# Kernel tuning notes

Measured on AMD Instinct MI355X. Metric: run time of the kernel, lower is better.

Reference implementation:

```python
import jax, jax.numpy as jnp
import numpy as np

N_PREV = 250_000   # rows of `features` / `coors` (voxels at previous scale)
N_FULL = 500_000   # full raw points (coors_inv_full / scale_coors_inv length)
V = 65_536         # voxels at current scale
C_IN = 64
C_OUT = 64
SCALE = 2
EPS = 1e-5


def lrelu(x):
    return jnp.where(x > 0, x, 0.1 * x)


def masked_bn(x, mask, gamma, beta):
    # training-mode BatchNorm1d over valid (non-padded) rows only; mask: [M,1]
    n = jnp.maximum(mask.sum(), 1.0)
    mu = (x * mask).sum(0) / n
    var = (((x - mu) * mask) ** 2).sum(0) / n  # biased var, as torch BN
    return gamma * (x - mu) * jax.lax.rsqrt(var + EPS) + beta


def setup_inputs():
    key = jax.random.key(0)
    ks = jax.random.split(key, 16)
    features = jax.random.normal(ks[0], (N_PREV, C_IN), jnp.float32)
    batch = jax.random.randint(ks[1], (N_PREV, 1), 0, 4)
    xy = jax.random.randint(ks[2], (N_PREV, 2), 0, 1000)
    z = jax.random.randint(ks[3], (N_PREV, 1), 0, 60)
    coors = jnp.concatenate([batch, xy, z], axis=1).astype(jnp.int32)
    coors_inv_full = jax.random.randint(ks[4], (N_FULL,), 0, N_PREV, jnp.int32)
    scale_coors_inv = jax.random.randint(ks[5], (N_FULL,), 0, V, jnp.int32)

    def lin(k, i, o):
        return jax.random.normal(k, (i, o), jnp.float32) / np.sqrt(i).astype(np.float32)

    h = C_OUT // 2
    return dict(
        features=features, coors=coors, coors_inv_full=coors_inv_full,
        scale_coors_inv=scale_coors_inv,
        W_in=lin(ks[6], C_IN, C_OUT), b_in=jnp.zeros((C_OUT,), jnp.float32),
        W1=lin(ks[7], C_IN, h), b1=jnp.zeros((h,), jnp.float32),
        g1=jnp.ones((h,), jnp.float32), be1=jnp.zeros((h,), jnp.float32),
        W2=lin(ks[8], h, h), b2=jnp.zeros((h,), jnp.float32),
        g2=jnp.ones((h,), jnp.float32), be2=jnp.zeros((h,), jnp.float32),
        W3=lin(ks[9], h, C_OUT), b3=jnp.zeros((C_OUT,), jnp.float32),
        Wo1=lin(ks[10], 2 * C_OUT, C_OUT), bo1=jnp.zeros((C_OUT,), jnp.float32),
        Wo2=lin(ks[11], C_OUT, C_OUT), bo2=jnp.zeros((C_OUT,), jnp.float32),
    )


def reference(features, coors, coors_inv_full, scale_coors_inv,
              W_in, b_in, W1, b1, g1, be1, W2, b2, g2, be2, W3, b3,
              Wo1, bo1, Wo2, bo2):
    # --- downsample: unique voxel key + scatter_mean (torch.unique return_inverse) ---
    b = coors[:, 0].astype(jnp.int32)
    xyz = coors[:, 1:].astype(jnp.int32) // SCALE
    keys = ((b * 501 + xyz[:, 0]) * 501 + xyz[:, 1]) * 31 + xyz[:, 2]  # < 2^31
    _, inv = jnp.unique(keys, return_inverse=True, size=N_PREV,
                        fill_value=jnp.int32(2**31 - 1))
    cnt = jax.ops.segment_sum(jnp.ones((N_PREV,), jnp.float32), inv,
                              num_segments=N_PREV)
    pooled = jax.ops.segment_sum(features, inv, num_segments=N_PREV) \
        / jnp.maximum(cnt, 1.0)[:, None]
    valid = (cnt > 0).astype(jnp.float32)[:, None]

    # --- identity branch: layer_in ---
    identity = lrelu(features @ W_in + b_in)

    # --- PPmodel on pooled voxels, then gather back by inv ---
    h = masked_bn(lrelu(pooled @ W1 + b1), valid, g1, be1)
    h = masked_bn(lrelu(h @ W2 + b2), valid, g2, be2)
    h = lrelu(h @ W3 + b3)
    out = jnp.concatenate([identity, h[inv]], axis=1)  # [N_PREV, 2*C_OUT]

    # --- gather to full points, layer_out, scatter_mean to scale voxels ---
    gathered = out[coors_inv_full]                      # [N_FULL, 2*C_OUT]
    po = lrelu(gathered @ Wo1 + bo1) @ Wo2 + bo2        # [N_FULL, C_OUT]
    cnt_v = jax.ops.segment_sum(jnp.ones((N_FULL,), jnp.float32),
                                scale_coors_inv, num_segments=V)
    v_feat = jax.ops.segment_sum(po, scale_coors_inv, num_segments=V) \
        / jnp.maximum(cnt_v, 1.0)[:, None]
    return v_feat
```

## Files before the change

kernel.cpp:

```cpp
#include <hip/hip_runtime.h>

#define N_PREV 250000
#define N_FULL 500000
#define NVOX   65536
#define NWORDS (1u<<20)
#define EPSF   1e-5f

typedef __attribute__((ext_vector_type(4)))  short short4v;
typedef __attribute__((ext_vector_type(8)))  short short8v;
typedef __attribute__((ext_vector_type(16))) float f32x16;

__device__ __forceinline__ float lrelu(float x){ return x > 0.0f ? x : 0.1f*x; }
__device__ __forceinline__ short f2bf_rne(float v){
    unsigned u = __float_as_uint(v);
    unsigned r = (u + 0x7fffu + ((u>>16)&1u)) >> 16;
    return (short)r;
}
__device__ __forceinline__ float bf2f(short s){
    return __uint_as_float(((unsigned)(unsigned short)s) << 16);
}

#define OFF_BITMAP   0ul
#define OFF_STATS    4194304ul
#define OFF_CNT      4195328ul
#define OFF_VH       5195328ul
#define OFF_Y        5457472ul
#define ZERO_BYTES   21457472ul
#define OFF_P2       37457472ul
#define OFF_PREF     69457472ul
#define OFF_BSUM     73651776ul
#define OFF_BOFF     73655872ul
#define OFF_UCNT     73659968ul
#define OFF_INV      73660224ul
#define OFF_P1       74660224ul
#define OFF_X2       106660224ul
#define WS_NEEDED    138660224ul
#define OFF_CSRJ     0ul
#define OFF_CSRH     2000000ul
#define OFF_VSTART   69457472ul
#define OFF_VNEXT    (OFF_VSTART+262400ul)
#define OFF_VPART    (OFF_VNEXT+262144ul)
#define OFF_VBSUM    (OFF_VPART+262144ul)

__device__ __forceinline__ int voxel_key(int4 c){
    return ((c.x*501 + (c.y>>1))*501 + (c.z>>1))*31 + (c.w>>1);
}

__global__ void k_mark(const int* __restrict__ coors, unsigned* __restrict__ bitmap){
    int i = blockIdx.x*256 + threadIdx.x;
    if(i >= N_PREV) return;
    int4 c = ((const int4*)coors)[i];
    int key = voxel_key(c);
    atomicOr(&bitmap[key>>5], 1u<<(key&31));
}

__global__ void __launch_bounds__(1024) k_scanA(const unsigned* __restrict__ bitmap,
                                                unsigned* __restrict__ pref,
                                                unsigned* __restrict__ bsum){
    __shared__ unsigned sh[1024];
    int tid = threadIdx.x;
    int w = blockIdx.x*1024 + tid;
    unsigned p = __popc(bitmap[w]);
    sh[tid] = p; __syncthreads();
    for(int off=1; off<1024; off<<=1){
        unsigned v = (tid>=off) ? sh[tid-off] : 0u;
        __syncthreads();
        sh[tid] += v;
        __syncthreads();
    }
    pref[w] = sh[tid] - p;
    if(tid==1023) bsum[blockIdx.x] = sh[tid];
}

__global__ void __launch_bounds__(1024) k_scanB(const unsigned* __restrict__ bsum,
                                                unsigned* __restrict__ boff,
                                                unsigned* __restrict__ Ucnt){
    __shared__ unsigned sh[1024];
    int tid = threadIdx.x;
    unsigned p = bsum[tid];
    sh[tid] = p; __syncthreads();
    for(int off=1; off<1024; off<<=1){
        unsigned v = (tid>=off) ? sh[tid-off] : 0u;
        __syncthreads();
        sh[tid] += v;
        __syncthreads();
    }
    boff[tid] = sh[tid] - p;
    if(tid==1023) Ucnt[0] = sh[tid];
}

__global__ void k_vhist(const int* __restrict__ scv, unsigned* __restrict__ vh){
    int p = blockIdx.x*256 + threadIdx.x;
    if(p < N_FULL) atomicAdd(&vh[scv[p]], 1u);
}

__global__ void __launch_bounds__(1024) k_vscanA(const unsigned* __restrict__ vh,
                                                 unsigned* __restrict__ vpart,
                                                 unsigned* __restrict__ vbsum){
    __shared__ unsigned sh[1024];
    int tid = threadIdx.x;
    int w = blockIdx.x*1024 + tid;
    unsigned p = vh[w];
    sh[tid] = p; __syncthreads();
    for(int off=1; off<1024; off<<=1){
        unsigned v = (tid>=off) ? sh[tid-off] : 0u;
        __syncthreads();
        sh[tid] += v;
        __syncthreads();
    }
    vpart[w] = sh[tid] - p;
    if(tid==1023) vbsum[blockIdx.x] = sh[tid];
}

__global__ void k_vscanB(unsigned* __restrict__ vbsum){
    int l = threadIdx.x;
    unsigned v = vbsum[l], orig = v;
    for(int off=1; off<64; off<<=1){
        unsigned o = __shfl_up(v, off);
        if(l>=off) v += o;
    }
    vbsum[l] = v - orig;
}

__global__ void __launch_bounds__(1024) k_vfix(const unsigned* __restrict__ vpart,
                                               const unsigned* __restrict__ vbsum,
                                               unsigned* __restrict__ vstart,
                                               unsigned* __restrict__ vnext){
    int w = blockIdx.x*1024 + threadIdx.x;
    unsigned s = vpart[w] + vbsum[w>>10];
    vstart[w] = s; vnext[w] = s;
    if(w == NVOX-1) vstart[NVOX] = N_FULL;
}

__global__ void k_fill(const int* __restrict__ cif, const int* __restrict__ scv,
                       const int* __restrict__ inv, unsigned* __restrict__ vnext,
                       int* __restrict__ csr_j, int* __restrict__ csr_h){
    int p = blockIdx.x*256 + threadIdx.x;
    if(p >= N_FULL) return;
    int jp = cif[p];
    unsigned pos = atomicAdd(&vnext[scv[p]], 1u);
    csr_j[pos] = jp;
    csr_h[pos] = inv[jp];
}

__global__ void __launch_bounds__(256) k_p1f(const float* __restrict__ feat,
        const int* __restrict__ coors, const unsigned* __restrict__ bitmap,
        const unsigned* __restrict__ pref, const unsigned* __restrict__ boff,
        const float* __restrict__ Win, const float* __restrict__ bin,
        const float* __restrict__ Wo1, const float* __restrict__ W1,
        unsigned short* __restrict__ P1, int* __restrict__ inv,
        float* __restrict__ cnt, unsigned short* __restrict__ yb){
    __shared__ __align__(16) short Ah[64*68];
    __shared__ __align__(16) short Al[64*68];
    __shared__ float ysh[64][33];
    __shared__ int rksh[64];
    int tid = threadIdx.x;
    int wave = tid >> 6, l = tid & 63;
    int g = l >> 5, c = l & 31;
    int rowhalf = (wave >> 1) * 32, colhalf = (wave & 1) * 32;

    {
        int col = tid >> 2, kseg = (tid & 3) * 16;
        short hi[16], lo[16];
        #pragma unroll
        for(int j=0;j<16;++j){
            float v = Win[(kseg+j)*64 + col];
            short h = f2bf_rne(v);
            hi[j] = h; lo[j] = f2bf_rne(v - bf2f(h));
        }
        #pragma unroll
        for(int i=0;i<4;++i){
            *(short4v*)&Ah[col*68 + kseg + 4*i] = *(short4v*)&hi[4*i];
            *(short4v*)&Al[col*68 + kseg + 4*i] = *(short4v*)&lo[4*i];
        }
    }
    __syncthreads();
    short8v w1h[4], w1l[4];
    #pragma unroll
    for(int s=0;s<4;++s){
        int base = (colhalf + c)*68 + s*16 + g*4;
        ((short4v*)&w1h[s])[0] = *(short4v*)&Ah[base];
        ((short4v*)&w1h[s])[1] = *(short4v*)&Ah[base + 8];
        ((short4v*)&w1l[s])[0] = *(short4v*)&Al[base];
        ((short4v*)&w1l[s])[1] = *(short4v*)&Al[base + 8];
    }
    __syncthreads();
    {
        int col = tid >> 2, kseg = (tid & 3) * 16;
        short hi[16];
        #pragma unroll
        for(int j=0;j<16;++j) hi[j] = f2bf_rne(Wo1[(kseg+j)*64 + col]);
        #pragma unroll
        for(int i=0;i<4;++i)
            *(short4v*)&Ah[col*68 + kseg + 4*i] = *(short4v*)&hi[4*i];
    }
    __syncthreads();
    short8v w2h[4];
    #pragma unroll
    for(int s=0;s<4;++s){
        int base = (colhalf + c)*68 + s*16 + g*4;
        ((short4v*)&w2h[s])[0] = *(short4v*)&Ah[base];
        ((short4v*)&w2h[s])[1] = *(short4v*)&Ah[base + 8];
    }
    __syncthreads();
    if(tid < 128){
        int col = tid >> 2, kseg = (tid & 3) * 16;
        short hi[16], lo[16];
        #pragma unroll
        for(int j=0;j<16;++j){
            float v = W1[(kseg+j)*32 + col];
            short h = f2bf_rne(v);
            hi[j] = h; lo[j] = f2bf_rne(v - bf2f(h));
        }
        #pragma unroll
        for(int i=0;i<4;++i){
            *(short4v*)&Ah[col*68 + kseg + 4*i] = *(short4v*)&hi[4*i];
            *(short4v*)&Al[col*68 + kseg + 4*i] = *(short4v*)&lo[4*i];
        }
    }
    __syncthreads();
    short8v w0h[4], w0l[4];
    #pragma unroll
    for(int s=0;s<4;++s){
        int base = c*68 + s*16 + g*4;
        ((short4v*)&w0h[s])[0] = *(short4v*)&Ah[base];
        ((short4v*)&w0h[s])[1] = *(short4v*)&Ah[base + 8];
        ((short4v*)&w0l[s])[0] = *(short4v*)&Al[base];
        ((short4v*)&w0l[s])[1] = *(short4v*)&Al[base + 8];
    }
    __syncthreads();

    float bc1 = bin[colhalf + c];

    const int NT = (N_PREV + 63) / 64;
    for(int tile = blockIdx.x; tile < NT; tile += gridDim.x){
        int rbase = tile * 64;
        {
            int row = tid >> 2, kseg = (tid & 3) * 16;
            int grow = rbase + row;
            float fv[16];
            if(grow < N_PREV){
                const float4* fp = (const float4*)&feat[grow*64 + kseg];
                *(float4*)&fv[0]  = fp[0];
                *(float4*)&fv[4]  = fp[1];
                *(float4*)&fv[8]  = fp[2];
                *(float4*)&fv[12] = fp[3];
            } else {
                #pragma unroll
                for(int j=0;j<16;++j) fv[j]=0.f;
            }
            short hi[16], lo[16];
            #pragma unroll
            for(int j=0;j<16;++j){
                short h = f2bf_rne(fv[j]);
                hi[j] = h; lo[j] = f2bf_rne(fv[j] - bf2f(h));
            }
            #pragma unroll
            for(int i=0;i<4;++i){
                *(short4v*)&Ah[row*68 + kseg + 4*i] = *(short4v*)&hi[4*i];
                *(short4v*)&Al[row*68 + kseg + 4*i] = *(short4v*)&lo[4*i];
            }
        }
        if(tid < 64){
            int grow = rbase + tid;
            if(grow < N_PREV){
                int4 c4 = ((const int4*)coors)[grow];
                int key = voxel_key(c4);
                int w = key>>5, b = key&31;
                int rank = (int)(boff[w>>10] + pref[w]) + __popc(bitmap[w] & ((1u<<b)-1u));
                rksh[tid] = rank;
                inv[grow] = rank;
                atomicAdd(&cnt[rank], 1.0f);
            } else rksh[tid] = -1;
        }
        __syncthreads();
        f32x16 acc;
        #pragma unroll
        for(int i=0;i<16;++i) acc[i]=0.f;
        #pragma unroll
        for(int s=0;s<4;++s){
            int abase = (rowhalf + c)*68 + s*16 + g*4;
            short8v ah, al;
            ((short4v*)&ah)[0] = *(short4v*)&Ah[abase];
            ((short4v*)&ah)[1] = *(short4v*)&Ah[abase + 8];
            ((short4v*)&al)[0] = *(short4v*)&Al[abase];
            ((short4v*)&al)[1] = *(short4v*)&Al[abase + 8];
            acc = __builtin_amdgcn_mfma_f32_32x32x16_bf16(ah, w1h[s], acc, 0,0,0);
            acc = __builtin_amdgcn_mfma_f32_32x32x16_bf16(al, w1h[s], acc, 0,0,0);
            acc = __builtin_amdgcn_mfma_f32_32x32x16_bf16(ah, w1l[s], acc, 0,0,0);
        }
        f32x16 accY;
        #pragma unroll
        for(int i=0;i<16;++i) accY[i]=0.f;
        if(wave < 2){
            #pragma unroll
            for(int s=0;s<4;++s){
                int abase = (wave*32 + c)*68 + s*16 + g*4;
                short8v ah, al;
                ((short4v*)&ah)[0] = *(short4v*)&Ah[abase];
                ((short4v*)&ah)[1] = *(short4v*)&Ah[abase + 8];
                ((short4v*)&al)[0] = *(short4v*)&Al[abase];
                ((short4v*)&al)[1] = *(short4v*)&Al[abase + 8];
                accY = __builtin_amdgcn_mfma_f32_32x32x16_bf16(ah, w0h[s], accY, 0,0,0);
                accY = __builtin_amdgcn_mfma_f32_32x32x16_bf16(al, w0h[s], accY, 0,0,0);
                accY = __builtin_amdgcn_mfma_f32_32x32x16_bf16(ah, w0l[s], accY, 0,0,0);
            }
        }
        __syncthreads();
        #pragma unroll
        for(int r=0;r<16;++r){
            int row = rowhalf + (r&3) + 8*(r>>2) + 4*g;
            float v = acc[r] + bc1;
            v = v > 0.f ? v : 0.1f*v;
            Ah[row*68 + colhalf + c] = f2bf_rne(v);
        }
        if(wave < 2){
            #pragma unroll
            for(int r=0;r<16;++r){
                int row = wave*32 + (r&3) + 8*(r>>2) + 4*g;
                ysh[row][c] = accY[r];
            }
        }
        __syncthreads();
        f32x16 acc2;
        #pragma unroll
        for(int i=0;i<16;++i) acc2[i]=0.f;
        #pragma unroll
        for(int s=0;s<4;++s){
            int abase = (rowhalf + c)*68 + s*16 + g*4;
            short8v ah;
            ((short4v*)&ah)[0] = *(short4v*)&Ah[abase];
            ((short4v*)&ah)[1] = *(short4v*)&Ah[abase + 8];
            acc2 = __builtin_amdgcn_mfma_f32_32x32x16_bf16(ah, w2h[s], acc2, 0,0,0);
        }
        #pragma unroll
        for(int r=0;r<16;++r){
            int grow = rbase + rowhalf + (r&3) + 8*(r>>2) + 4*g;
            if(grow < N_PREV) P1[grow*64 + colhalf + c] = (unsigned short)f2bf_rne(acc2[r]);
        }
        #pragma unroll
        for(int q=0;q<4;++q){
            int e = q*256 + tid;
            int row = e >> 4, pr = e & 15;
            int rk = rksh[row];
            if(rk >= 0){
                unsigned h0 = (unsigned)(unsigned short)f2bf_rne(ysh[row][2*pr]);
                unsigned h1 = (unsigned)(unsigned short)f2bf_rne(ysh[row][2*pr+1]);
                unsigned pk = h0 | (h1 << 16);
                unsigned short* addr = yb + (size_t)rk*32 + 2*pr;
                asm volatile("global_atomic_pk_add_bf16 %0, %1, off"
                             :: "v"(addr), "v"(pk) : "memory");
            }
        }
        __syncthreads();
    }
}

__global__ void __launch_bounds__(256) k_bn1(const unsigned short* __restrict__ yb,
        const float* __restrict__ cnt, const unsigned* __restrict__ Ucnt,
        const float* __restrict__ b1, float* __restrict__ stats){
    __shared__ float sst[32], qst[32];
    int tid = threadIdx.x;
    if(tid < 32){ sst[tid]=0.f; qst[tid]=0.f; }
    __syncthreads();
    int U = (int)Ucnt[0];
    int total = U*4;
    int c8 = (tid&3)*8;
    float bb[8];
    #pragma unroll
    for(int j=0;j<8;++j) bb[j] = b1[c8+j];
    float s[8], q[8];
    #pragma unroll
    for(int j=0;j<8;++j){ s[j]=0.f; q[j]=0.f; }
    for(int e = blockIdx.x*256 + tid; e < total; e += gridDim.x*256){
        int row = e >> 2;
        float rv = 1.0f/cnt[row];
        uint4 a = ((const uint4*)yb)[e];
        unsigned wv[4] = {a.x,a.y,a.z,a.w};
        #pragma unroll
        for(int k=0;k<4;++k){
            float lo = __uint_as_float(wv[k]<<16);
            float hi = __uint_as_float(wv[k]&0xffff0000u);
            float v0 = lrelu(lo*rv + bb[2*k]);
            float v1 = lrelu(hi*rv + bb[2*k+1]);
            s[2*k]+=v0; q[2*k]+=v0*v0;
            s[2*k+1]+=v1; q[2*k+1]+=v1*v1;
        }
    }
    #pragma unroll
    for(int j=0;j<8;++j){ atomicAdd(&sst[c8+j], s[j]); atomicAdd(&qst[c8+j], q[j]); }
    __syncthreads();
    if(tid < 32){ atomicAdd(&stats[tid], sst[tid]); atomicAdd(&stats[32+tid], qst[tid]); }
}

__global__ void k_bnfin(const unsigned* __restrict__ Ucnt, const float* __restrict__ g,
                        float* __restrict__ stats, int off){
    int c = threadIdx.x;
    if(c>=32) return;
    float n = (float)max(Ucnt[0], 1u);
    float mu = stats[off+c]/n;
    float var = stats[off+32+c]/n - mu*mu;
    stats[off+64+c] = mu;
    stats[off+96+c] = g[c]*rsqrtf(var + EPSF);
}

__global__ void __launch_bounds__(256) k_ppm2(const unsigned short* __restrict__ yb,
        const float* __restrict__ cnt, const unsigned* __restrict__ Ucnt,
        const float* __restrict__ W2, const float* __restrict__ b1i,
        const float* __restrict__ b2, const float* __restrict__ be1,
        unsigned short* __restrict__ x2b, float* __restrict__ stats){
    __shared__ __align__(16) short Ah[128*36];
    __shared__ __align__(16) short Al[128*36];
    __shared__ float ash[32], bbsh[32], b1sh[32];
    __shared__ float red[4][64];
    int tid = threadIdx.x;
    int wave = tid >> 6, l = tid & 63;
    int g = l >> 5, c = l & 31;

    if(tid < 32){
        float mu=stats[64+tid], sc=stats[96+tid];
        ash[tid]=sc; bbsh[tid]=be1[tid]-mu*sc;
        b1sh[tid]=b1i[tid];
    }
    if(tid >= 64 && tid < 128){
        int t = tid - 64;
        int col = t >> 1, kseg = (t & 1) * 16;
        short hi[16], lo[16];
        #pragma unroll
        for(int j=0;j<16;++j){
            float v = W2[(kseg+j)*32 + col];
            short h = f2bf_rne(v);
            hi[j] = h; lo[j] = f2bf_rne(v - bf2f(h));
        }
        #pragma unroll
        for(int i=0;i<4;++i){
            *(short4v*)&Ah[col*36 + kseg + 4*i] = *(short4v*)&hi[4*i];
            *(short4v*)&Al[col*36 + kseg + 4*i] = *(short4v*)&lo[4*i];
        }
    }
    __syncthreads();
    short8v wh[2], wl[2];
    #pragma unroll
    for(int s=0;s<2;++s){
        int base = c*36 + s*16 + g*4;
        ((short4v*)&wh[s])[0] = *(short4v*)&Ah[base];
        ((short4v*)&wh[s])[1] = *(short4v*)&Ah[base + 8];
        ((short4v*)&wl[s])[0] = *(short4v*)&Al[base];
        ((short4v*)&wl[s])[1] = *(short4v*)&Al[base + 8];
    }
    __syncthreads();

    int U = (int)Ucnt[0];
    float bc = b2[c];
    float s_acc = 0.f, q_acc = 0.f;

    const int NT = (N_PREV + 127) / 128;
    for(int tile = blockIdx.x; tile < NT; tile += gridDim.x){
        int rbase = tile * 128;
        if(rbase >= U) break;
        {
            int row = tid >> 1, kseg = (tid & 1) * 16;
            int grow = rbase + row;
            float fv[16];
            if(grow < U){
                float rv = 1.0f/cnt[grow];
                uint4 a0 = *(const uint4*)&yb[grow*32 + kseg];
                uint4 a1 = *(const uint4*)&yb[grow*32 + kseg + 8];
                unsigned wv[8] = {a0.x,a0.y,a0.z,a0.w,a1.x,a1.y,a1.z,a1.w};
                #pragma unroll
                for(int k=0;k<8;++k){
                    float lo = __uint_as_float(wv[k]<<16);
                    float hi = __uint_as_float(wv[k]&0xffff0000u);
                    float v0 = lrelu(lo*rv + b1sh[kseg+2*k]);
                    float v1 = lrelu(hi*rv + b1sh[kseg+2*k+1]);
                    fv[2*k]   = v0*ash[kseg+2*k]   + bbsh[kseg+2*k];
                    fv[2*k+1] = v1*ash[kseg+2*k+1] + bbsh[kseg+2*k+1];
                }
            } else {
                #pragma unroll
                for(int j=0;j<16;++j) fv[j]=0.f;
            }
            short hi[16], lo[16];
            #pragma unroll
            for(int j=0;j<16;++j){
                short h = f2bf_rne(fv[j]);
                hi[j] = h; lo[j] = f2bf_rne(fv[j] - bf2f(h));
            }
            #pragma unroll
            for(int i=0;i<4;++i){
                *(short4v*)&Ah[row*36 + kseg + 4*i] = *(short4v*)&hi[4*i];
                *(short4v*)&Al[row*36 + kseg + 4*i] = *(short4v*)&lo[4*i];
            }
        }
        __syncthreads();
        f32x16 acc;
        #pragma unroll
        for(int i=0;i<16;++i) acc[i]=0.f;
        #pragma unroll
        for(int s=0;s<2;++s){
            int abase = (wave*32 + c)*36 + s*16 + g*4;
            short8v ah, al;
            ((short4v*)&ah)[0] = *(short4v*)&Ah[abase];
            ((short4v*)&ah)[1] = *(short4v*)&Ah[abase + 8];
            ((short4v*)&al)[0] = *(short4v*)&Al[abase];
            ((short4v*)&al)[1] = *(short4v*)&Al[abase + 8];
            acc = __builtin_amdgcn_mfma_f32_32x32x16_bf16(ah, wh[s], acc, 0,0,0);
            acc = __builtin_amdgcn_mfma_f32_32x32x16_bf16(al, wh[s], acc, 0,0,0);
            acc = __builtin_amdgcn_mfma_f32_32x32x16_bf16(ah, wl[s], acc, 0,0,0);
        }
        #pragma unroll
        for(int r=0;r<16;++r){
            int rl = wave*32 + (r&3) + 8*(r>>2) + 4*g;
            int grow = rbase + rl;
            if(grow < U){
                float v = acc[r] + bc;
                v = v > 0.f ? v : 0.1f*v;
                x2b[grow*32 + c] = (unsigned short)f2bf_rne(v);
                s_acc += v; q_acc += v*v;
            }
        }
        __syncthreads();
    }
    s_acc += __shfl_xor(s_acc, 32);
    q_acc += __shfl_xor(q_acc, 32);
    if(l < 32){ red[wave][c] = s_acc; red[wave][32+c] = q_acc; }
    __syncthreads();
    if(tid < 64){
        float t = red[0][tid]+red[1][tid]+red[2][tid]+red[3][tid];
        atomicAdd(&stats[128+tid], t);
    }
}

__global__ void __launch_bounds__(256) k_ppm3(const unsigned short* __restrict__ x2b,
        const unsigned* __restrict__ Ucnt, const float* __restrict__ W3,
        const float* __restrict__ b3, const float* __restrict__ be2,
        const float* __restrict__ Wo1, unsigned short* __restrict__ P2,
        const float* __restrict__ stats){
    __shared__ __align__(16) short Ah[64*36];
    __shared__ __align__(16) short Al[64*36];
    __shared__ __align__(16) short Ih[64*68];
    __shared__ __align__(16) short Il[64*36];
    __shared__ float ash[32], bbsh[32];
    int tid = threadIdx.x;
    int wave = tid >> 6, l = tid & 63;
    int g = l >> 5, c = l & 31;
    int rowhalf = (wave >> 1) * 32, colhalf = (wave & 1) * 32;

    if(tid < 32){
        float mu=stats[192+tid], sc=stats[224+tid];
        ash[tid]=sc; bbsh[tid]=be2[tid]-mu*sc;
    }
    if(tid >= 128){
        int t = tid - 128;
        int col = t >> 1, kseg = (t & 1) * 16;
        short hi[16], lo[16];
        #pragma unroll
        for(int j=0;j<16;++j){
            float v = W3[(kseg+j)*64 + col];
            short h = f2bf_rne(v);
            hi[j] = h; lo[j] = f2bf_rne(v - bf2f(h));
        }
        #pragma unroll
        for(int i=0;i<4;++i){
            *(short4v*)&Ih[col*36 + kseg + 4*i] = *(short4v*)&hi[4*i];
            *(short4v*)&Il[col*36 + kseg + 4*i] = *(short4v*)&lo[4*i];
        }
    }
    __syncthreads();
    short8v w3h[2], w3l[2];
    #pragma unroll
    for(int s=0;s<2;++s){
        int base = (colhalf + c)*36 + s*16 + g*4;
        ((short4v*)&w3h[s])[0] = *(short4v*)&Ih[base];
        ((short4v*)&w3h[s])[1] = *(short4v*)&Ih[base + 8];
        ((short4v*)&w3l[s])[0] = *(short4v*)&Il[base];
        ((short4v*)&w3l[s])[1] = *(short4v*)&Il[base + 8];
    }
    __syncthreads();
    {
        int col = tid >> 2, kseg = (tid & 3) * 16;
        short hi[16];
        #pragma unroll
        for(int j=0;j<16;++j) hi[j] = f2bf_rne(Wo1[4096 + (kseg+j)*64 + col]);
        #pragma unroll
        for(int i=0;i<4;++i)
            *(short4v*)&Ih[col*68 + kseg + 4*i] = *(short4v*)&hi[4*i];
    }
    __syncthreads();
    short8v w2h[4];
    #pragma unroll
    for(int s=0;s<4;++s){
        int base = (colhalf + c)*68 + s*16 + g*4;
        ((short4v*)&w2h[s])[0] = *(short4v*)&Ih[base];
        ((short4v*)&w2h[s])[1] = *(short4v*)&Ih[base + 8];
    }
    __syncthreads();

    int U = (int)Ucnt[0];
    float bc3 = b3[colhalf + c];

    const int NT = (N_PREV + 63) / 64;
    for(int tile = blockIdx.x; tile < NT; tile += gridDim.x){
        int rbase = tile * 64;
        if(rbase >= U) break;
        if(tid < 128){
            int row = tid >> 1, kseg = (tid & 1) * 16;
            int grow = rbase + row;
            float fv[16];
            if(grow < U){
                uint4 a0 = *(const uint4*)&x2b[grow*32 + kseg];
                uint4 a1 = *(const uint4*)&x2b[grow*32 + kseg + 8];
                unsigned wv[8] = {a0.x,a0.y,a0.z,a0.w,a1.x,a1.y,a1.z,a1.w};
                #pragma unroll
                for(int k=0;k<8;++k){
                    float lo = __uint_as_float(wv[k]<<16);
                    float hi = __uint_as_float(wv[k]&0xffff0000u);
                    fv[2*k]   = lo*ash[kseg+2*k]   + bbsh[kseg+2*k];
                    fv[2*k+1] = hi*ash[kseg+2*k+1] + bbsh[kseg+2*k+1];
                }
            } else {
                #pragma unroll
                for(int j=0;j<16;++j) fv[j]=0.f;
            }
            short hi[16], lo[16];
            #pragma unroll
            for(int j=0;j<16;++j){
                short h = f2bf_rne(fv[j]);
                hi[j] = h; lo[j] = f2bf_rne(fv[j] - bf2f(h));
            }
            #pragma unroll
            for(int i=0;i<4;++i){
                *(short4v*)&Ah[row*36 + kseg + 4*i] = *(short4v*)&hi[4*i];
                *(short4v*)&Al[row*36 + kseg + 4*i] = *(short4v*)&lo[4*i];
            }
        }
        __syncthreads();
        f32x16 acc;
        #pragma unroll
        for(int i=0;i<16;++i) acc[i]=0.f;
        #pragma unroll
        for(int s=0;s<2;++s){
            int abase = (rowhalf + c)*36 + s*16 + g*4;
            short8v ah, al;
            ((short4v*)&ah)[0] = *(short4v*)&Ah[abase];
            ((short4v*)&ah)[1] = *(short4v*)&Ah[abase + 8];
            ((short4v*)&al)[0] = *(short4v*)&Al[abase];
            ((short4v*)&al)[1] = *(short4v*)&Al[abase + 8];
            acc = __builtin_amdgcn_mfma_f32_32x32x16_bf16(ah, w3h[s], acc, 0,0,0);
            acc = __builtin_amdgcn_mfma_f32_32x32x16_bf16(al, w3h[s], acc, 0,0,0);
            acc = __builtin_amdgcn_mfma_f32_32x32x16_bf16(ah, w3l[s], acc, 0,0,0);
        }
        #pragma unroll
        for(int r=0;r<16;++r){
            int row = rowhalf + (r&3) + 8*(r>>2) + 4*g;
            float v = acc[r] + bc3;
            v = v > 0.f ? v : 0.1f*v;
            Ih[row*68 + colhalf + c] = f2bf_rne(v);
        }
        __syncthreads();
        f32x16 acc2;
        #pragma unroll
        for(int i=0;i<16;++i) acc2[i]=0.f;
        #pragma unroll
        for(int s=0;s<4;++s){
            int abase = (rowhalf + c)*68 + s*16 + g*4;
            short8v ah;
            ((short4v*)&ah)[0] = *(short4v*)&Ih[abase];
            ((short4v*)&ah)[1] = *(short4v*)&Ih[abase + 8];
            acc2 = __builtin_amdgcn_mfma_f32_32x32x16_bf16(ah, w2h[s], acc2, 0,0,0);
        }
        #pragma unroll
        for(int r=0;r<16;++r){
            int grow = rbase + rowhalf + (r&3) + 8*(r>>2) + 4*g;
            if(grow < U) P2[grow*64 + colhalf + c] = (unsigned short)f2bf_rne(acc2[r]);
        }
        __syncthreads();
    }
}

__global__ void __launch_bounds__(256) k_vox(const unsigned* __restrict__ vstart,
        const int* __restrict__ csr_j, const int* __restrict__ csr_h,
        const unsigned short* __restrict__ P1, const unsigned short* __restrict__ P2,
        const float* __restrict__ bo1, const float* __restrict__ Wo2,
        const float* __restrict__ bo2, float* __restrict__ out){
    __shared__ float tsh[4][64];
    int tid = threadIdx.x;
    int wib = tid>>6, lane = tid&63;
    float wreg[64];
    #pragma unroll
    for(int k=0;k<64;++k) wreg[k] = Wo2[k*64+lane];
    float b1c = bo1[lane], b2c = bo2[lane];
    int wglobal = blockIdx.x*4 + wib;
    for(int vq=0; vq<4; ++vq){
        int vox = wglobal*4 + vq;
        int s = (int)vstart[vox], e = (int)vstart[vox+1];
        float acc = 0.f;
        for(int i=s; i<e; i+=64){
            int n = min(e-i, 64);
            int jv=0, hv=0;
            if(lane<n){ jv = csr_j[i+lane]; hv = csr_h[i+lane]; }
            for(int q0=0; q0<n; q0+=8){
                float pa[8], pb[8];
                #pragma unroll
                for(int t=0;t<8;++t){
                    int qq = q0 + t;
                    qq = (qq < n) ? qq : q0;
                    int j = __shfl(jv, qq);
                    int h = __shfl(hv, qq);
                    pa[t] = bf2f((short)P1[(size_t)j*64 + lane]);
                    pb[t] = bf2f((short)P2[(size_t)h*64 + lane]);
                }
                #pragma unroll
                for(int t=0;t<8;++t){
                    if(q0 + t < n){
                        float g = pa[t] + pb[t] + b1c;
                        acc += (g>0.f) ? g : 0.1f*g;
                    }
                }
            }
        }
        tsh[wib][lane] = acc;
        float dot = 0.f;
        const float4* t4 = (const float4*)tsh[wib];
        #pragma unroll
        for(int k4=0;k4<16;++k4){
            float4 t = t4[k4];
            dot += t.x*wreg[4*k4] + t.y*wreg[4*k4+1] + t.z*wreg[4*k4+2] + t.w*wreg[4*k4+3];
        }
        float cntv = (float)(e - s);
        out[vox*64+lane] = (dot + cntv*b2c) / fmaxf(cntv, 1.f);
    }
}

extern "C" void kernel_launch(void* const* d_in, const int* in_sizes, int n_in,
                              void* d_out, int out_size, void* d_ws, size_t ws_size,
                              hipStream_t stream) {
    if(ws_size < WS_NEEDED) return;

    const float* features = (const float*)d_in[0];
    const int*   coors    = (const int*)d_in[1];
    const int*   cif      = (const int*)d_in[2];
    const int*   scv      = (const int*)d_in[3];
    const float* W_in     = (const float*)d_in[4];
    const float* b_in     = (const float*)d_in[5];
    const float* W1       = (const float*)d_in[6];
    const float* b1       = (const float*)d_in[7];
    const float* g1       = (const float*)d_in[8];
    const float* be1      = (const float*)d_in[9];
    const float* W2       = (const float*)d_in[10];
    const float* b2       = (const float*)d_in[11];
    const float* g2       = (const float*)d_in[12];
    const float* be2      = (const float*)d_in[13];
    const float* W3       = (const float*)d_in[14];
    const float* b3       = (const float*)d_in[15];
    const float* Wo1      = (const float*)d_in[16];
    const float* bo1      = (const float*)d_in[17];
    const float* Wo2      = (const float*)d_in[18];
    const float* bo2      = (const float*)d_in[19];

    char* ws = (char*)d_ws;
    unsigned* bitmap = (unsigned*)(ws + OFF_BITMAP);
    float*    stats  = (float*)(ws + OFF_STATS);
    float*    cnt    = (float*)(ws + OFF_CNT);
    unsigned* vh     = (unsigned*)(ws + OFF_VH);
    unsigned short* yb = (unsigned short*)(ws + OFF_Y);
    unsigned short* P2 = (unsigned short*)(ws + OFF_P2);
    unsigned* pref   = (unsigned*)(ws + OFF_PREF);
    unsigned* bsum   = (unsigned*)(ws + OFF_BSUM);
    unsigned* boff   = (unsigned*)(ws + OFF_BOFF);
    unsigned* Ucnt   = (unsigned*)(ws + OFF_UCNT);
    int*      inv    = (int*)(ws + OFF_INV);
    unsigned short* P1 = (unsigned short*)(ws + OFF_P1);
    unsigned short* x2b = (unsigned short*)(ws + OFF_X2);
    int*      csr_j  = (int*)(ws + OFF_CSRJ);
    int*      csr_h  = (int*)(ws + OFF_CSRH);
    unsigned* vstart = (unsigned*)(ws + OFF_VSTART);
    unsigned* vnext  = (unsigned*)(ws + OFF_VNEXT);
    unsigned* vpart  = (unsigned*)(ws + OFF_VPART);
    unsigned* vbsum  = (unsigned*)(ws + OFF_VBSUM);

    hipMemsetAsync(d_ws, 0, ZERO_BYTES, stream);

    k_mark  <<<(N_PREV+255)/256, 256, 0, stream>>>(coors, bitmap);
    k_scanA <<<1024, 1024, 0, stream>>>(bitmap, pref, bsum);
    k_scanB <<<1, 1024, 0, stream>>>(bsum, boff, Ucnt);
    k_p1f   <<<1024, 256, 0, stream>>>(features, coors, bitmap, pref, boff,
                                       W_in, b_in, Wo1, W1, P1, inv, cnt, yb);
    k_vhist <<<(N_FULL+255)/256, 256, 0, stream>>>(scv, vh);
    k_vscanA<<<64, 1024, 0, stream>>>(vh, vpart, vbsum);
    k_vscanB<<<1, 64, 0, stream>>>(vbsum);
    k_vfix  <<<64, 1024, 0, stream>>>(vpart, vbsum, vstart, vnext);
    k_fill  <<<(N_FULL+255)/256, 256, 0, stream>>>(cif, scv, inv, vnext, csr_j, csr_h);
    k_bn1   <<<1024, 256, 0, stream>>>(yb, cnt, Ucnt, b1, stats);
    k_bnfin <<<1, 32, 0, stream>>>(Ucnt, g1, stats, 0);
    k_ppm2  <<<1024, 256, 0, stream>>>(yb, cnt, Ucnt, W2, b1, b2, be1, x2b, stats);
    k_bnfin <<<1, 32, 0, stream>>>(Ucnt, g2, stats, 128);
    k_ppm3  <<<1024, 256, 0, stream>>>(x2b, Ucnt, W3, b3, be2, Wo1, P2, stats);
    k_vox   <<<NVOX/16, 256, 0, stream>>>(vstart, csr_j, csr_h, P1, P2, bo1, Wo2, bo2, (float*)d_out);
}
```

Measured before the change: 279.7 us.

## Split Wo2 projection out of k_vox into separate split-bf16 MFMA GEMM kernel

The per-voxel Wo2 matvec, previously done with a 64-register weight array and LDS broadcast inside the gather kernel, moves to a new kernel. k_vox now writes the summed pre-projection activations to a workspace buffer T, and k_wo2 runs a tiled 64x64 GEMM using bf16 MFMA with a hi/lo split (three products) to keep near-fp32 accuracy. This is meant to cut register pressure in k_vox and raise its occupancy, at the cost of an extra 16MB round trip and one more launch. The k_p1f grid is also doubled.

```diff
diff --git a/kernel.cpp b/kernel.cpp
--- a/kernel.cpp
+++ b/kernel.cpp
@@ -26,6 +26,7 @@
 #define OFF_VH       5195328ul
 #define OFF_Y        5457472ul
 #define ZERO_BYTES   21457472ul
+#define OFF_T        5457472ul
 #define OFF_P2       37457472ul
 #define OFF_PREF     69457472ul
 #define OFF_BSUM     73651776ul
@@ -681,15 +682,10 @@
 __global__ void __launch_bounds__(256) k_vox(const unsigned* __restrict__ vstart,
         const int* __restrict__ csr_j, const int* __restrict__ csr_h,
         const unsigned short* __restrict__ P1, const unsigned short* __restrict__ P2,
-        const float* __restrict__ bo1, const float* __restrict__ Wo2,
-        const float* __restrict__ bo2, float* __restrict__ out){
-    __shared__ float tsh[4][64];
+        const float* __restrict__ bo1, float* __restrict__ T){
     int tid = threadIdx.x;
     int wib = tid>>6, lane = tid&63;
-    float wreg[64];
-    #pragma unroll
-    for(int k=0;k<64;++k) wreg[k] = Wo2[k*64+lane];
-    float b1c = bo1[lane], b2c = bo2[lane];
+    float b1c = bo1[lane];
     int wglobal = blockIdx.x*4 + wib;
     for(int vq=0; vq<4; ++vq){
         int vox = wglobal*4 + vq;
@@ -719,16 +715,102 @@
                 }
             }
         }
-        tsh[wib][lane] = acc;
-        float dot = 0.f;
-        const float4* t4 = (const float4*)tsh[wib];
-        #pragma unroll
-        for(int k4=0;k4<16;++k4){
-            float4 t = t4[k4];
-            dot += t.x*wreg[4*k4] + t.y*wreg[4*k4+1] + t.z*wreg[4*k4+2] + t.w*wreg[4*k4+3];
-        }
-        float cntv = (float)(e - s);
-        out[vox*64+lane] = (dot + cntv*b2c) / fmaxf(cntv, 1.f);
+        T[(size_t)vox*64 + lane] = acc;
+    }
+}
+
+__global__ void __launch_bounds__(256) k_wo2(const float* __restrict__ T,
+        const unsigned* __restrict__ vstart, const float* __restrict__ Wo2,
+        const float* __restrict__ bo2, float* __restrict__ out){
+    __shared__ __align__(16) short Ah[64*68];
+    __shared__ __align__(16) short Al[64*68];
+    __shared__ float csh[64];
+    int tid = threadIdx.x;
+    int wave = tid >> 6, l = tid & 63;
+    int g = l >> 5, c = l & 31;
+    int rowhalf = (wave >> 1) * 32, colhalf = (wave & 1) * 32;
+
+    {
+        int col = tid >> 2, kseg = (tid & 3) * 16;
+        short hi[16], lo[16];
+        #pragma unroll
+        for(int j=0;j<16;++j){
+            float v = Wo2[(kseg+j)*64 + col];
+            short h = f2bf_rne(v);
+            hi[j] = h; lo[j] = f2bf_rne(v - bf2f(h));
+        }
+        #pragma unroll
+        for(int i=0;i<4;++i){
+            *(short4v*)&Ah[col*68 + kseg + 4*i] = *(short4v*)&hi[4*i];
+            *(short4v*)&Al[col*68 + kseg + 4*i] = *(short4v*)&lo[4*i];
+        }
+    }
+    __syncthreads();
+    short8v wh[4], wl[4];
+    #pragma unroll
+    for(int s=0;s<4;++s){
+        int base = (colhalf + c)*68 + s*16 + g*4;
+        ((short4v*)&wh[s])[0] = *(short4v*)&Ah[base];
+        ((short4v*)&wh[s])[1] = *(short4v*)&Ah[base + 8];
+        ((short4v*)&wl[s])[0] = *(short4v*)&Al[base];
+        ((short4v*)&wl[s])[1] = *(short4v*)&Al[base + 8];
+    }
+    __syncthreads();
+
+    float bo2c = bo2[colhalf + c];
+
+    const int NT = NVOX / 64;
+    for(int tile = blockIdx.x; tile < NT; tile += gridDim.x){
+        int rbase = tile * 64;
+        {
+            int row = tid >> 2, kseg = (tid & 3) * 16;
+            const float4* fp = (const float4*)&T[(size_t)(rbase + row)*64 + kseg];
+            float fv[16];
+            *(float4*)&fv[0]  = fp[0];
+            *(float4*)&fv[4]  = fp[1];
+            *(float4*)&fv[8]  = fp[2];
+            *(float4*)&fv[12] = fp[3];
+            short hi[16], lo[16];
+            #pragma unroll
+            for(int j=0;j<16;++j){
+                short h = f2bf_rne(fv[j]);
+                hi[j] = h; lo[j] = f2bf_rne(fv[j] - bf2f(h));
+            }
+            #pragma unroll
+            for(int i=0;i<4;++i){
+                *(short4v*)&Ah[row*68 + kseg + 4*i] = *(short4v*)&hi[4*i];
+                *(short4v*)&Al[row*68 + kseg + 4*i] = *(short4v*)&lo[4*i];
+            }
+        }
+        if(tid < 64){
+            int vox = rbase + tid;
+            csh[tid] = (float)(vstart[vox+1] - vstart[vox]);
+        }
+        __syncthreads();
+        f32x16 acc;
+        #pragma unroll
+        for(int i=0;i<16;++i) acc[i]=0.f;
+        #pragma unroll
+        for(int s=0;s<4;++s){
+            int abase = (rowhalf + c)*68 + s*16 + g*4;
+            short8v ah, al;
+            ((short4v*)&ah)[0] = *(short4v*)&Ah[abase];
+            ((short4v*)&ah)[1] = *(short4v*)&Ah[abase + 8];
+            ((short4v*)&al)[0] = *(short4v*)&Al[abase];
+            ((short4v*)&al)[1] = *(short4v*)&Al[abase + 8];
+            acc = __builtin_amdgcn_mfma_f32_32x32x16_bf16(ah, wh[s], acc, 0,0,0);
+            acc = __builtin_amdgcn_mfma_f32_32x32x16_bf16(al, wh[s], acc, 0,0,0);
+            acc = __builtin_amdgcn_mfma_f32_32x32x16_bf16(ah, wl[s], acc, 0,0,0);
+        }
+        #pragma unroll
+        for(int r=0;r<16;++r){
+            int row = rowhalf + (r&3) + 8*(r>>2) + 4*g;
+            float cv = csh[row];
+            float rv = (cv > 0.f) ? 1.0f/cv : 0.f;
+            float bz = (cv > 0.f) ? bo2c : 0.f;
+            out[(size_t)(rbase + row)*64 + colhalf + c] = acc[r]*rv + bz;
+        }
+        __syncthreads();
     }
 }
 
@@ -764,6 +846,7 @@
     float*    cnt    = (float*)(ws + OFF_CNT);
     unsigned* vh     = (unsigned*)(ws + OFF_VH);
     unsigned short* yb = (unsigned short*)(ws + OFF_Y);
+    float*    T      = (float*)(ws + OFF_T);
     unsigned short* P2 = (unsigned short*)(ws + OFF_P2);
     unsigned* pref   = (unsigned*)(ws + OFF_PREF);
     unsigned* bsum   = (unsigned*)(ws + OFF_BSUM);
@@ -784,7 +867,7 @@
     k_mark  <<<(N_PREV+255)/256, 256, 0, stream>>>(coors, bitmap);
     k_scanA <<<1024, 1024, 0, stream>>>(bitmap, pref, bsum);
     k_scanB <<<1, 1024, 0, stream>>>(bsum, boff, Ucnt);
-    k_p1f   <<<1024, 256, 0, stream>>>(features, coors, bitmap, pref, boff,
+    k_p1f   <<<2048, 256, 0, stream>>>(features, coors, bitmap, pref, boff,
                                        W_in, b_in, Wo1, W1, P1, inv, cnt, yb);
     k_vhist <<<(N_FULL+255)/256, 256, 0, stream>>>(scv, vh);
     k_vscanA<<<64, 1024, 0, stream>>>(vh, vpart, vbsum);
@@ -796,5 +879,6 @@
     k_ppm2  <<<1024, 256, 0, stream>>>(yb, cnt, Ucnt, W2, b1, b2, be1, x2b, stats);
     k_bnfin <<<1, 32, 0, stream>>>(Ucnt, g2, stats, 128);
     k_ppm3  <<<1024, 256, 0, stream>>>(x2b, Ucnt, W3, b3, be2, Wo1, P2, stats);
-    k_vox   <<<NVOX/16, 256, 0, stream>>>(vstart, csr_j, csr_h, P1, P2, bo1, Wo2, bo2, (float*)d_out);
-}
+    k_vox   <<<NVOX/16, 256, 0, stream>>>(vstart, csr_j, csr_h, P1, P2, bo1, T);
+    k_wo2   <<<1024, 256, 0, stream>>>(T, vstart, Wo2, bo2, (float*)d_out);
+}
```

Result: no change. 284.5 us (+1.7%).
